# Optimization experiments

Hardware: AMD Instinct MI355X
Metric: run time of the kernel (lower is better)

The kernel has to match this reference:

```python
import jax, jax.numpy as jnp
import numpy as np

NHEAD = 16

def setup_inputs() -> dict:
    key = jax.random.key(0)
    ks = jax.random.split(key, 7)
    b, l, d = 4, 2048, 1024
    s = 1.0 / np.sqrt(d)
    return {
        "Q": jax.random.normal(ks[0], (b, l, d), jnp.float32),
        "K": jax.random.normal(ks[1], (b, l, d), jnp.float32),
        "V": jax.random.normal(ks[2], (b, l, d), jnp.float32),
        "WQ": jax.random.normal(ks[3], (d, d), jnp.float32) * s,
        "WK": jax.random.normal(ks[4], (d, d), jnp.float32) * s,
        "WV": jax.random.normal(ks[5], (d, d), jnp.float32) * s,
        "WO": jax.random.normal(ks[6], (d, d), jnp.float32) * s,
    }

def reference(Q, K, V, WQ, WK, WV, WO):
    # WQ/WK/WV/WO stored torch-style as [out, in]; Linear(x) = x @ W.T
    b, lq, d = Q.shape
    lk = K.shape[1]
    h = NHEAD
    dk = d // h
    # project and split heads: [b, l, h, dk]
    q = (Q @ WQ.T).reshape(b, lq, h, dk)
    k = (K @ WK.T).reshape(b, lk, h, dk)
    v = (V @ WV.T).reshape(b, lk, h, dk)
    # scaled dot-product attention (dropout = identity in eval mode)
    scale = 1.0 / jnp.sqrt(jnp.asarray(dk, Q.dtype))
    score = jnp.einsum('bqhd,bkhd->bhqk', q, k) * scale  # [b,h,lq,lk]
    attn = jax.nn.softmax(score, axis=-1)
    o = jnp.einsum('bhqk,bkhd->bqhd', attn, v).reshape(b, lq, h * dk)
    return o @ WO.T
```

## Files before the change

### kernel.cpp

```cpp
#include <hip/hip_runtime.h>
#include <stdint.h>

#define D_MODEL 1024
#define NHEADS 16
#define DKH 64
#define SEQ 2048
#define BATCH 4
#define M_TOT (BATCH * SEQ)
#define LOG2E 1.44269504088896340736f

typedef __bf16 v8bf __attribute__((ext_vector_type(8)));
typedef __bf16 v4bf __attribute__((ext_vector_type(4)));
typedef _Float16 v8h __attribute__((ext_vector_type(8)));
typedef _Float16 v4h __attribute__((ext_vector_type(4)));
typedef float v4f __attribute__((ext_vector_type(4)));
typedef float v16f __attribute__((ext_vector_type(16)));
typedef unsigned int v4u __attribute__((ext_vector_type(4)));
typedef unsigned int v2u __attribute__((ext_vector_type(2)));

typedef const __attribute__((address_space(1))) void* gas_ptr;
typedef __attribute__((address_space(3))) void* las_ptr;

static __device__ __forceinline__ void async16(const void* g, void* l) {
    __builtin_amdgcn_global_load_lds((gas_ptr)g, (las_ptr)l, 16, 0, 0);
}

static __device__ __forceinline__ v4f mfma16x32(v8bf a, v8bf b, v4f c) {
    return __builtin_amdgcn_mfma_f32_16x16x32_bf16(a, b, c, 0, 0, 0);
}
static __device__ __forceinline__ v16f mfma32x16bf(v8bf a, v8bf b, v16f c) {
    return __builtin_amdgcn_mfma_f32_32x32x16_bf16(a, b, c, 0, 0, 0);
}
static __device__ __forceinline__ v16f mfma32x16h(v8h a, v8h b, v16f c) {
    return __builtin_amdgcn_mfma_f32_32x32x16_f16(a, b, c, 0, 0, 0);
}
static __device__ __forceinline__ unsigned pkh(float a, float b) {
    return __builtin_bit_cast(unsigned, __builtin_amdgcn_cvt_pkrtz(a, b));
}
static __device__ __forceinline__ void plswap(unsigned& x, unsigned& y) {
    v2u r = __builtin_amdgcn_permlane32_swap(x, y, false, false);
    x = r[0];
    y = r[1];
}
static __device__ __forceinline__ float fexp2(float x) {
#if __has_builtin(__builtin_amdgcn_exp2f)
    return __builtin_amdgcn_exp2f(x);
#else
    float r;
    asm("v_exp_f32 %0, %1" : "=v"(r) : "v"(x));
    return r;
#endif
}

__global__ __launch_bounds__(256) void cvt_x(const float* __restrict__ src,
                                             __bf16* __restrict__ dst) {
    int i = blockIdx.x * 256 + threadIdx.x;
    const float4* s = (const float4*)src;
    float4 a = s[2 * i], b = s[2 * i + 1];
    v8bf o;
    o[0] = (__bf16)a.x; o[1] = (__bf16)a.y; o[2] = (__bf16)a.z; o[3] = (__bf16)a.w;
    o[4] = (__bf16)b.x; o[5] = (__bf16)b.y; o[6] = (__bf16)b.z; o[7] = (__bf16)b.w;
    *(v8bf*)(dst + (size_t)i * 8) = o;
}

__global__ __launch_bounds__(256) void cvt_x3(const float* __restrict__ s0,
                                              const float* __restrict__ s1,
                                              const float* __restrict__ s2,
                                              __bf16* __restrict__ d0,
                                              __bf16* __restrict__ d1,
                                              __bf16* __restrict__ d2) {
    int t = blockIdx.x >> 12;
    int i = (blockIdx.x & 4095) * 256 + threadIdx.x;
    const float* src = (t == 0) ? s0 : (t == 1) ? s1 : s2;
    __bf16* dst = (t == 0) ? d0 : (t == 1) ? d1 : d2;
    const float4* s = (const float4*)src;
    float4 a = s[2 * i], b = s[2 * i + 1];
    v8bf o;
    o[0] = (__bf16)a.x; o[1] = (__bf16)a.y; o[2] = (__bf16)a.z; o[3] = (__bf16)a.w;
    o[4] = (__bf16)b.x; o[5] = (__bf16)b.y; o[6] = (__bf16)b.z; o[7] = (__bf16)b.w;
    *(v8bf*)(dst + (size_t)i * 8) = o;
}

__global__ __launch_bounds__(256) void cvt_w(const float* __restrict__ w0,
                                             const float* __restrict__ w1,
                                             const float* __restrict__ w2,
                                             const float* __restrict__ w3,
                                             __bf16* __restrict__ dst) {
    int gid = blockIdx.x * 256 + threadIdx.x;
    int tsel = gid >> 17;
    int off = gid & 131071;
    const float* s = (tsel == 0) ? w0 : (tsel == 1) ? w1 : (tsel == 2) ? w2 : w3;
    const float4* sp = (const float4*)s + 2 * (size_t)off;
    float4 a = sp[0], b = sp[1];
    v8bf o;
    o[0] = (__bf16)a.x; o[1] = (__bf16)a.y; o[2] = (__bf16)a.z; o[3] = (__bf16)a.w;
    o[4] = (__bf16)b.x; o[5] = (__bf16)b.y; o[6] = (__bf16)b.z; o[7] = (__bf16)b.w;
    *(v8bf*)(dst + ((size_t)tsel << 20) + (size_t)off * 8) = o;
}

#define GEMM_KLOOP(Abase, Wbase)                                                   \
    auto stage = [&](int bi, int k0) {                                             \
        _Pragma("unroll") for (int p = 0; p < 2; ++p) {                            \
            int rb = (p * 4 + wave) * 16;                                          \
            async16(Abase + (size_t)(rb + wrow) * D_MODEL + k0, &As[bi][rb * 32]); \
            async16(Wbase + (size_t)(rb + wrow) * D_MODEL + k0, &Bs[bi][rb * 32]); \
        }                                                                          \
    };                                                                             \
    stage(0, 0);                                                                   \
    for (int it = 0; it < D_MODEL / 32; ++it) {                                    \
        const int cur = it & 1;                                                    \
        if (it + 1 < D_MODEL / 32) {                                               \
            stage(cur ^ 1, (it + 1) * 32);                                         \
            asm volatile("s_waitcnt vmcnt(4)" ::: "memory");                       \
        } else {                                                                   \
            asm volatile("s_waitcnt vmcnt(0)" ::: "memory");                       \
        }                                                                          \
        __builtin_amdgcn_s_barrier();                                              \
        __builtin_amdgcn_sched_barrier(0);                                         \
        v8bf af[4], bfr[4];                                                        \
        _Pragma("unroll") for (int mt = 0; mt < 4; ++mt)                           \
            af[mt] = *(const v8bf*)&As[cur][(mw + mt * 16 + r) * 32 + rdpos];      \
        _Pragma("unroll") for (int nt = 0; nt < 4; ++nt)                           \
            bfr[nt] = *(const v8bf*)&Bs[cur][(nw + nt * 16 + r) * 32 + rdpos];     \
        _Pragma("unroll") for (int mt = 0; mt < 4; ++mt)                           \
            _Pragma("unroll") for (int nt = 0; nt < 4; ++nt)                       \
                acc[mt][nt] = mfma16x32(af[mt], bfr[nt], acc[mt][nt]);             \
        asm volatile("s_waitcnt lgkmcnt(0)" ::: "memory");                         \
        __builtin_amdgcn_s_barrier();                                              \
    }

template <int LAYOUT>
__global__ __launch_bounds__(256) void gemm_nt(const __bf16* __restrict__ A,
                                               const __bf16* __restrict__ W,
                                               void* __restrict__ Cv, float scale) {
    const int t = threadIdx.x, lane = t & 63, wave = t >> 6;
    const int r = lane & 15, qd = lane >> 4;
    const int m0 = blockIdx.x * 128, n0 = blockIdx.y * 128;
    const int mw = (wave & 1) * 64, nw = (wave >> 1) * 64;

    __shared__ __align__(16) __bf16 As[2][128 * 32];
    __shared__ __align__(16) __bf16 Bs[2][128 * 32];

    const int wc = (lane & 3) ^ ((lane >> 3) & 3);
    const int wrow = lane >> 2;
    const int rdpos = (qd ^ ((r >> 1) & 3)) * 8;

    const __bf16* Ab = A + (size_t)m0 * D_MODEL + wc * 8;
    const __bf16* Wb = W + (size_t)n0 * D_MODEL + wc * 8;

    v4f acc[4][4] = {};
    GEMM_KLOOP(Ab, Wb)

#pragma unroll
    for (int mt = 0; mt < 4; ++mt)
#pragma unroll
        for (int nt = 0; nt < 4; ++nt) {
            int row = m0 + mw + mt * 16 + qd * 4;
            int col = n0 + nw + nt * 16 + r;
            if (LAYOUT == 0) {
                float* C = (float*)Cv;
#pragma unroll
                for (int i = 0; i < 4; ++i)
                    C[(size_t)(row + i) * D_MODEL + col] = acc[mt][nt][i];
            } else {
                int bb = row >> 11, l = row & (SEQ - 1);
                int h = col >> 6, d = col & (DKH - 1);
                if (LAYOUT == 2) {
                    _Float16* vt = (_Float16*)Cv;
                    v4h o;
#pragma unroll
                    for (int i = 0; i < 4; ++i) o[i] = (_Float16)acc[mt][nt][i];
                    *(v4h*)&vt[((size_t)((bb * NHEADS + h) * DKH + d)) * SEQ + l] = o;
                } else {
                    __bf16* dst = (__bf16*)Cv;
#pragma unroll
                    for (int i = 0; i < 4; ++i)
                        dst[(((size_t)(bb * NHEADS + h) * SEQ) + l + i) * DKH + d] =
                            (__bf16)(acc[mt][nt][i] * scale);
                }
            }
        }
}

__global__ __launch_bounds__(256) void gemm_qkv(const __bf16* __restrict__ xq,
                                                const __bf16* __restrict__ xk,
                                                const __bf16* __restrict__ xv,
                                                const __bf16* __restrict__ wb,
                                                __bf16* __restrict__ qh,
                                                __bf16* __restrict__ kh,
                                                _Float16* __restrict__ vtb, float qs) {
    const int z = blockIdx.z;
    const __bf16* A = (z == 0) ? xq : (z == 1) ? xk : xv;
    const __bf16* W = wb + (size_t)z * D_MODEL * D_MODEL;

    const int t = threadIdx.x, lane = t & 63, wave = t >> 6;
    const int r = lane & 15, qd = lane >> 4;
    const int m0 = blockIdx.x * 128, n0 = blockIdx.y * 128;
    const int mw = (wave & 1) * 64, nw = (wave >> 1) * 64;

    __shared__ __align__(16) __bf16 As[2][128 * 32];
    __shared__ __align__(16) __bf16 Bs[2][128 * 32];

    const int wc = (lane & 3) ^ ((lane >> 3) & 3);
    const int wrow = lane >> 2;
    const int rdpos = (qd ^ ((r >> 1) & 3)) * 8;

    const __bf16* Ab = A + (size_t)m0 * D_MODEL + wc * 8;
    const __bf16* Wb = W + (size_t)n0 * D_MODEL + wc * 8;

    v4f acc[4][4] = {};
    GEMM_KLOOP(Ab, Wb)

    const float scale = (z == 0) ? qs : 1.0f;
#pragma unroll
    for (int mt = 0; mt < 4; ++mt)
#pragma unroll
        for (int nt = 0; nt < 4; ++nt) {
            int row = m0 + mw + mt * 16 + qd * 4;
            int col = n0 + nw + nt * 16 + r;
            int bb = row >> 11, l = row & (SEQ - 1);
            int h = col >> 6, d = col & (DKH - 1);
            if (z == 2) {
                v4h o;
#pragma unroll
                for (int i = 0; i < 4; ++i) o[i] = (_Float16)acc[mt][nt][i];
                *(v4h*)&vtb[((size_t)((bb * NHEADS + h) * DKH + d)) * SEQ + l] = o;
            } else {
                __bf16* dst = (z == 0) ? qh : kh;
#pragma unroll
                for (int i = 0; i < 4; ++i)
                    dst[(((size_t)(bb * NHEADS + h) * SEQ) + l + i) * DKH + d] =
                        (__bf16)(acc[mt][nt][i] * scale);
            }
        }
}

__global__ __launch_bounds__(256, 2) void attn_kernel(const __bf16* __restrict__ qh,
                                                      const __bf16* __restrict__ kh,
                                                      const _Float16* __restrict__ vt,
                                                      __bf16* __restrict__ oh) {
    const int lane = threadIdx.x & 63, wave = threadIdx.x >> 6;
    const int l31 = lane & 31, hi = lane >> 5, l7 = lane & 7;
    const int id = blockIdx.x;
    const int bh = (id & 7) * 8 + ((id >> 3) & 7);
    const int q0 = (id >> 6) * 256 + wave * 64;

    __shared__ __align__(16) __bf16 Kb[2][64 * 64];
    __shared__ __align__(16) _Float16 Vb[2][64 * 64];

    const __bf16* kbh = kh + (size_t)bh * SEQ * DKH;
    const _Float16* vbh = vt + (size_t)bh * DKH * SEQ;

    v8bf qf[2][4];
#pragma unroll
    for (int qa = 0; qa < 2; ++qa)
#pragma unroll
        for (int c = 0; c < 4; ++c)
            qf[qa][c] = *(const v8bf*)&qh[((size_t)bh * SEQ + q0 + qa * 32 + l31) * DKH +
                                          c * 16 + hi * 8];

    v16f oacc[2][2] = {};
    float ps[2] = {0.f, 0.f};
    const v16f dz = {};

    const int srow = lane >> 3;
    const int sc = (lane & 7) ^ srow;

#pragma unroll
    for (int p = 0; p < 2; ++p) {
        int rb = wave * 16 + p * 8;
        async16(kbh + (size_t)(rb + srow) * DKH + sc * 8, &Kb[0][rb * 64]);
        async16(vbh + (size_t)(rb + srow) * SEQ + sc * 8, &Vb[0][rb * 64]);
    }

    for (int tt = 0; tt < SEQ / 64; ++tt) {
        const int buf = tt & 1;
        __syncthreads();
        if (tt + 1 < SEQ / 64) {
            const int t0 = (tt + 1) * 64;
#pragma unroll
            for (int p = 0; p < 2; ++p) {
                int rb = wave * 16 + p * 8;
                async16(kbh + (size_t)(t0 + rb + srow) * DKH + sc * 8, &Kb[buf ^ 1][rb * 64]);
                async16(vbh + (size_t)(rb + srow) * SEQ + t0 + sc * 8, &Vb[buf ^ 1][rb * 64]);
            }
        }
        const __bf16* Kc = Kb[buf];
        const _Float16* Vc = Vb[buf];
#pragma unroll
        for (int kb = 0; kb < 2; ++kb) {
            v8bf ka[4];
#pragma unroll
            for (int c = 0; c < 4; ++c)
                ka[c] = *(const v8bf*)&Kc[(kb * 32 + l31) * 64 + (((c * 2 + hi) ^ l7) << 3)];
            v8h pb[2][2];
#pragma unroll
            for (int qa = 0; qa < 2; ++qa) {
                v16f d = mfma32x16bf(ka[0], qf[qa][0], dz);
#pragma unroll
                for (int c = 1; c < 4; ++c) d = mfma32x16bf(ka[c], qf[qa][c], d);
                float e[16];
#pragma unroll
                for (int i = 0; i < 16; ++i) e[i] = fexp2(d[i]);
                ps[qa] += (((e[0] + e[1]) + (e[2] + e[3])) + ((e[4] + e[5]) + (e[6] + e[7]))) +
                          (((e[8] + e[9]) + (e[10] + e[11])) + ((e[12] + e[13]) + (e[14] + e[15])));
#pragma unroll
                for (int kc = 0; kc < 2; ++kc) {
                    unsigned a0 = pkh(e[kc * 8 + 0], e[kc * 8 + 1]);
                    unsigned a1 = pkh(e[kc * 8 + 2], e[kc * 8 + 3]);
                    unsigned b0 = pkh(e[kc * 8 + 4], e[kc * 8 + 5]);
                    unsigned b1 = pkh(e[kc * 8 + 6], e[kc * 8 + 7]);
                    plswap(a0, b0);
                    plswap(a1, b1);
                    v4u w = {a0, a1, b0, b1};
                    pb[qa][kc] = __builtin_bit_cast(v8h, w);
                }
            }
#pragma unroll
            for (int dg = 0; dg < 2; ++dg)
#pragma unroll
                for (int kc = 0; kc < 2; ++kc) {
                    v8h va = *(const v8h*)&Vc[(dg * 32 + l31) * 64 +
                                              (((kb * 4 + kc * 2 + hi) ^ l7) << 3)];
#pragma unroll
                    for (int qa = 0; qa < 2; ++qa)
                        oacc[qa][dg] = mfma32x16h(va, pb[qa][kc], oacc[qa][dg]);
                }
        }
    }

    const int b = bh >> 4, h = bh & (NHEADS - 1);
#pragma unroll
    for (int qa = 0; qa < 2; ++qa) {
        float tot = ps[qa] + __shfl_xor(ps[qa], 32, 64);
        float inv = 1.0f / tot;
        int lq = q0 + qa * 32 + l31;
        __bf16* op = oh + (((size_t)(b * SEQ + lq)) * NHEADS + h) * DKH;
#pragma unroll
        for (int dg = 0; dg < 2; ++dg)
#pragma unroll
            for (int g = 0; g < 4; ++g) {
                v4bf ov;
#pragma unroll
                for (int i = 0; i < 4; ++i) ov[i] = (__bf16)(oacc[qa][dg][g * 4 + i] * inv);
                *(v4bf*)(op + dg * 32 + g * 8 + hi * 4) = ov;
            }
    }
}

extern "C" void kernel_launch(void* const* d_in, const int* in_sizes, int n_in,
                              void* d_out, int out_size, void* d_ws, size_t ws_size,
                              hipStream_t stream) {
    const float* Q = (const float*)d_in[0];
    const float* K = (const float*)d_in[1];
    const float* V = (const float*)d_in[2];
    const float* WQ = (const float*)d_in[3];
    const float* WK = (const float*)d_in[4];
    const float* WV = (const float*)d_in[5];
    const float* WO = (const float*)d_in[6];
    float* out = (float*)d_out;

    const size_t elems = (size_t)M_TOT * D_MODEL;
    const size_t welems = (size_t)D_MODEL * D_MODEL;
    const size_t fused_need = 8 * welems + 6 * 2 * elems;

    dim3 gg(M_TOT / 128, D_MODEL / 128);

    if (ws_size >= fused_need) {
        __bf16* wb = (__bf16*)d_ws;
        __bf16* xq = wb + 4 * welems;
        __bf16* xk = xq + elems;
        __bf16* xv = xk + elems;
        __bf16* qh = xv + elems;
        __bf16* kh = qh + elems;
        _Float16* vtb = (_Float16*)(kh + elems);
        __bf16* oh = xq;

        cvt_w<<<2048, 256, 0, stream>>>(WQ, WK, WV, WO, wb);
        cvt_x3<<<3 * 4096, 256, 0, stream>>>(Q, K, V, xq, xk, xv);
        dim3 gz(M_TOT / 128, D_MODEL / 128, 3);
        gemm_qkv<<<gz, 256, 0, stream>>>(xq, xk, xv, wb, qh, kh, vtb, 0.125f * LOG2E);
        attn_kernel<<<512, 256, 0, stream>>>(qh, kh, vtb, oh);
        gemm_nt<0><<<gg, 256, 0, stream>>>(oh, wb + 3 * welems, out, 1.0f);
    } else {
        __bf16* wb = (__bf16*)d_ws;
        __bf16* xb = wb + 4 * welems;
        __bf16* qh = xb + elems;
        __bf16* kh = qh + elems;
        _Float16* vtb = (_Float16*)(kh + elems);
        __bf16* oh = (__bf16*)(vtb + elems);

        cvt_w<<<2048, 256, 0, stream>>>(WQ, WK, WV, WO, wb);
        cvt_x<<<4096, 256, 0, stream>>>(Q, xb);
        gemm_nt<1><<<gg, 256, 0, stream>>>(xb, wb, qh, 0.125f * LOG2E);
        cvt_x<<<4096, 256, 0, stream>>>(K, xb);
        gemm_nt<1><<<gg, 256, 0, stream>>>(xb, wb + welems, kh, 1.0f);
        cvt_x<<<4096, 256, 0, stream>>>(V, xb);
        gemm_nt<2><<<gg, 256, 0, stream>>>(xb, wb + 2 * welems, vtb, 1.0f);
        attn_kernel<<<512, 256, 0, stream>>>(qh, kh, vtb, oh);
        gemm_nt<0><<<gg, 256, 0, stream>>>(oh, wb + 3 * welems, out, 1.0f);
    }
}
```

Baseline: 323.2 us.

## Halve per-wave query rows in attention and merge conversion kernels

The attention kernel now gives each wave 32 query rows instead of 64, doubling the grid from 512 to 1024 blocks so more blocks fill the device's compute units. The cost is that every K/V tile loaded into shared memory is reused across half as many queries, which doubles K/V traffic. The separate weight and activation fp32-to-bf16 conversion launches are also merged into a single cvt_all launch to save one kernel launch.

```diff
diff --git a/kernel.cpp b/kernel.cpp
--- a/kernel.cpp
+++ b/kernel.cpp
@@ -55,24 +55,6 @@
 __global__ __launch_bounds__(256) void cvt_x(const float* __restrict__ src,
                                              __bf16* __restrict__ dst) {
     int i = blockIdx.x * 256 + threadIdx.x;
-    const float4* s = (const float4*)src;
-    float4 a = s[2 * i], b = s[2 * i + 1];
-    v8bf o;
-    o[0] = (__bf16)a.x; o[1] = (__bf16)a.y; o[2] = (__bf16)a.z; o[3] = (__bf16)a.w;
-    o[4] = (__bf16)b.x; o[5] = (__bf16)b.y; o[6] = (__bf16)b.z; o[7] = (__bf16)b.w;
-    *(v8bf*)(dst + (size_t)i * 8) = o;
-}
-
-__global__ __launch_bounds__(256) void cvt_x3(const float* __restrict__ s0,
-                                              const float* __restrict__ s1,
-                                              const float* __restrict__ s2,
-                                              __bf16* __restrict__ d0,
-                                              __bf16* __restrict__ d1,
-                                              __bf16* __restrict__ d2) {
-    int t = blockIdx.x >> 12;
-    int i = (blockIdx.x & 4095) * 256 + threadIdx.x;
-    const float* src = (t == 0) ? s0 : (t == 1) ? s1 : s2;
-    __bf16* dst = (t == 0) ? d0 : (t == 1) ? d1 : d2;
     const float4* s = (const float4*)src;
     float4 a = s[2 * i], b = s[2 * i + 1];
     v8bf o;
@@ -96,6 +78,42 @@
     o[0] = (__bf16)a.x; o[1] = (__bf16)a.y; o[2] = (__bf16)a.z; o[3] = (__bf16)a.w;
     o[4] = (__bf16)b.x; o[5] = (__bf16)b.y; o[6] = (__bf16)b.z; o[7] = (__bf16)b.w;
     *(v8bf*)(dst + ((size_t)tsel << 20) + (size_t)off * 8) = o;
+}
+
+__global__ __launch_bounds__(256) void cvt_all(const float* __restrict__ Q,
+                                               const float* __restrict__ K,
+                                               const float* __restrict__ V,
+                                               const float* __restrict__ w0,
+                                               const float* __restrict__ w1,
+                                               const float* __restrict__ w2,
+                                               const float* __restrict__ w3,
+                                               __bf16* __restrict__ xq,
+                                               __bf16* __restrict__ xk,
+                                               __bf16* __restrict__ xv,
+                                               __bf16* __restrict__ wb) {
+    const int blk = blockIdx.x;
+    const float* src;
+    __bf16* dst;
+    size_t off8;
+    if (blk < 2048) {
+        int gid = blk * 256 + threadIdx.x;
+        int tsel = gid >> 17;
+        src = (tsel == 0) ? w0 : (tsel == 1) ? w1 : (tsel == 2) ? w2 : w3;
+        dst = wb + ((size_t)tsel << 20);
+        off8 = (size_t)(gid & 131071);
+    } else {
+        int gb = blk - 2048;
+        int t = gb >> 12;
+        src = (t == 0) ? Q : (t == 1) ? K : V;
+        dst = (t == 0) ? xq : (t == 1) ? xk : xv;
+        off8 = (size_t)((gb & 4095) * 256 + threadIdx.x);
+    }
+    const float4* sp = (const float4*)src + 2 * off8;
+    float4 a = sp[0], b = sp[1];
+    v8bf o;
+    o[0] = (__bf16)a.x; o[1] = (__bf16)a.y; o[2] = (__bf16)a.z; o[3] = (__bf16)a.w;
+    o[4] = (__bf16)b.x; o[5] = (__bf16)b.y; o[6] = (__bf16)b.z; o[7] = (__bf16)b.w;
+    *(v8bf*)(dst + off8 * 8) = o;
 }
 
 #define GEMM_KLOOP(Abase, Wbase)                                                   \
@@ -243,7 +261,7 @@
     const int l31 = lane & 31, hi = lane >> 5, l7 = lane & 7;
     const int id = blockIdx.x;
     const int bh = (id & 7) * 8 + ((id >> 3) & 7);
-    const int q0 = (id >> 6) * 256 + wave * 64;
+    const int q0 = (id >> 6) * 128 + wave * 32;
 
     __shared__ __align__(16) __bf16 Kb[2][64 * 64];
     __shared__ __align__(16) _Float16 Vb[2][64 * 64];
@@ -251,16 +269,13 @@
     const __bf16* kbh = kh + (size_t)bh * SEQ * DKH;
     const _Float16* vbh = vt + (size_t)bh * DKH * SEQ;
 
-    v8bf qf[2][4];
-#pragma unroll
-    for (int qa = 0; qa < 2; ++qa)
-#pragma unroll
-        for (int c = 0; c < 4; ++c)
-            qf[qa][c] = *(const v8bf*)&qh[((size_t)bh * SEQ + q0 + qa * 32 + l31) * DKH +
-                                          c * 16 + hi * 8];
-
-    v16f oacc[2][2] = {};
-    float ps[2] = {0.f, 0.f};
+    v8bf qf[4];
+#pragma unroll
+    for (int c = 0; c < 4; ++c)
+        qf[c] = *(const v8bf*)&qh[((size_t)bh * SEQ + q0 + l31) * DKH + c * 16 + hi * 8];
+
+    v16f oacc[2] = {};
+    float ps = 0.f;
     const v16f dz = {};
 
     const int srow = lane >> 3;
@@ -293,28 +308,25 @@
 #pragma unroll
             for (int c = 0; c < 4; ++c)
                 ka[c] = *(const v8bf*)&Kc[(kb * 32 + l31) * 64 + (((c * 2 + hi) ^ l7) << 3)];
-            v8h pb[2][2];
-#pragma unroll
-            for (int qa = 0; qa < 2; ++qa) {
-                v16f d = mfma32x16bf(ka[0], qf[qa][0], dz);
-#pragma unroll
-                for (int c = 1; c < 4; ++c) d = mfma32x16bf(ka[c], qf[qa][c], d);
-                float e[16];
-#pragma unroll
-                for (int i = 0; i < 16; ++i) e[i] = fexp2(d[i]);
-                ps[qa] += (((e[0] + e[1]) + (e[2] + e[3])) + ((e[4] + e[5]) + (e[6] + e[7]))) +
-                          (((e[8] + e[9]) + (e[10] + e[11])) + ((e[12] + e[13]) + (e[14] + e[15])));
-#pragma unroll
-                for (int kc = 0; kc < 2; ++kc) {
-                    unsigned a0 = pkh(e[kc * 8 + 0], e[kc * 8 + 1]);
-                    unsigned a1 = pkh(e[kc * 8 + 2], e[kc * 8 + 3]);
-                    unsigned b0 = pkh(e[kc * 8 + 4], e[kc * 8 + 5]);
-                    unsigned b1 = pkh(e[kc * 8 + 6], e[kc * 8 + 7]);
-                    plswap(a0, b0);
-                    plswap(a1, b1);
-                    v4u w = {a0, a1, b0, b1};
-                    pb[qa][kc] = __builtin_bit_cast(v8h, w);
-                }
+            v16f d = mfma32x16bf(ka[0], qf[0], dz);
+#pragma unroll
+            for (int c = 1; c < 4; ++c) d = mfma32x16bf(ka[c], qf[c], d);
+            float e[16];
+#pragma unroll
+            for (int i = 0; i < 16; ++i) e[i] = fexp2(d[i]);
+            ps += (((e[0] + e[1]) + (e[2] + e[3])) + ((e[4] + e[5]) + (e[6] + e[7]))) +
+                  (((e[8] + e[9]) + (e[10] + e[11])) + ((e[12] + e[13]) + (e[14] + e[15])));
+            v8h pb[2];
+#pragma unroll
+            for (int kc = 0; kc < 2; ++kc) {
+                unsigned a0 = pkh(e[kc * 8 + 0], e[kc * 8 + 1]);
+                unsigned a1 = pkh(e[kc * 8 + 2], e[kc * 8 + 3]);
+                unsigned b0 = pkh(e[kc * 8 + 4], e[kc * 8 + 5]);
+                unsigned b1 = pkh(e[kc * 8 + 6], e[kc * 8 + 7]);
+                plswap(a0, b0);
+                plswap(a1, b1);
+                v4u w = {a0, a1, b0, b1};
+                pb[kc] = __builtin_bit_cast(v8h, w);
             }
 #pragma unroll
             for (int dg = 0; dg < 2; ++dg)
@@ -322,30 +334,25 @@
                 for (int kc = 0; kc < 2; ++kc) {
                     v8h va = *(const v8h*)&Vc[(dg * 32 + l31) * 64 +
                                               (((kb * 4 + kc * 2 + hi) ^ l7) << 3)];
-#pragma unroll
-                    for (int qa = 0; qa < 2; ++qa)
-                        oacc[qa][dg] = mfma32x16h(va, pb[qa][kc], oacc[qa][dg]);
+                    oacc[dg] = mfma32x16h(va, pb[kc], oacc[dg]);
                 }
         }
     }
 
     const int b = bh >> 4, h = bh & (NHEADS - 1);
-#pragma unroll
-    for (int qa = 0; qa < 2; ++qa) {
-        float tot = ps[qa] + __shfl_xor(ps[qa], 32, 64);
-        float inv = 1.0f / tot;
-        int lq = q0 + qa * 32 + l31;
-        __bf16* op = oh + (((size_t)(b * SEQ + lq)) * NHEADS + h) * DKH;
-#pragma unroll
-        for (int dg = 0; dg < 2; ++dg)
-#pragma unroll
-            for (int g = 0; g < 4; ++g) {
-                v4bf ov;
-#pragma unroll
-                for (int i = 0; i < 4; ++i) ov[i] = (__bf16)(oacc[qa][dg][g * 4 + i] * inv);
-                *(v4bf*)(op + dg * 32 + g * 8 + hi * 4) = ov;
-            }
-    }
+    float tot = ps + __shfl_xor(ps, 32, 64);
+    float inv = 1.0f / tot;
+    int lq = q0 + l31;
+    __bf16* op = oh + (((size_t)(b * SEQ + lq)) * NHEADS + h) * DKH;
+#pragma unroll
+    for (int dg = 0; dg < 2; ++dg)
+#pragma unroll
+        for (int g = 0; g < 4; ++g) {
+            v4bf ov;
+#pragma unroll
+            for (int i = 0; i < 4; ++i) ov[i] = (__bf16)(oacc[dg][g * 4 + i] * inv);
+            *(v4bf*)(op + dg * 32 + g * 8 + hi * 4) = ov;
+        }
 }
 
 extern "C" void kernel_launch(void* const* d_in, const int* in_sizes, int n_in,
@@ -376,11 +383,10 @@
         _Float16* vtb = (_Float16*)(kh + elems);
         __bf16* oh = xq;
 
-        cvt_w<<<2048, 256, 0, stream>>>(WQ, WK, WV, WO, wb);
-        cvt_x3<<<3 * 4096, 256, 0, stream>>>(Q, K, V, xq, xk, xv);
+        cvt_all<<<14336, 256, 0, stream>>>(Q, K, V, WQ, WK, WV, WO, xq, xk, xv, wb);
         dim3 gz(M_TOT / 128, D_MODEL / 128, 3);
         gemm_qkv<<<gz, 256, 0, stream>>>(xq, xk, xv, wb, qh, kh, vtb, 0.125f * LOG2E);
-        attn_kernel<<<512, 256, 0, stream>>>(qh, kh, vtb, oh);
+        attn_kernel<<<1024, 256, 0, stream>>>(qh, kh, vtb, oh);
         gemm_nt<0><<<gg, 256, 0, stream>>>(oh, wb + 3 * welems, out, 1.0f);
     } else {
         __bf16* wb = (__bf16*)d_ws;
@@ -397,7 +403,7 @@
         gemm_nt<1><<<gg, 256, 0, stream>>>(xb, wb + welems, kh, 1.0f);
         cvt_x<<<4096, 256, 0, stream>>>(V, xb);
         gemm_nt<2><<<gg, 256, 0, stream>>>(xb, wb + 2 * welems, vtb, 1.0f);
-        attn_kernel<<<512, 256, 0, stream>>>(qh, kh, vtb, oh);
+        attn_kernel<<<1024, 256, 0, stream>>>(qh, kh, vtb, oh);
         gemm_nt<0><<<gg, 256, 0, stream>>>(oh, wb + 3 * welems, out, 1.0f);
     }
 }
```

New measurement: 344.1 us. 6.5% more time.
